# Kernel optimization log

Measured on AMD Instinct MI355X. Metric: run time of the kernel, lower is better.

The kernel has to match this reference:

```python
import jax, jax.numpy as jnp
import numpy as np

N = 50000      # ncount
IN_CH = 256    # in_channels
OUT_CH = 128   # out_channels
NNZ = 800000   # nnz per sparse matrix (avg degree 16)


def _spmm(rows, cols, vals, dense, n_rows):
    # sparse(COO) @ dense : gather rows of dense by col index, scale, scatter-add by row
    contrib = vals[:, None] * dense[cols]              # [nnz, F]
    return jax.ops.segment_sum(contrib, rows, num_segments=n_rows)


def setup_inputs() -> dict:
    key = jax.random.key(0)
    ks = jax.random.split(key, 12)
    phi_indices = jnp.stack([
        jax.random.randint(ks[0], (NNZ,), 0, N),
        jax.random.randint(ks[1], (NNZ,), 0, N)])
    phi_values = jax.random.normal(ks[2], (NNZ,), dtype=jnp.float32)
    phi_inverse_indices = jnp.stack([
        jax.random.randint(ks[3], (NNZ,), 0, N),
        jax.random.randint(ks[4], (NNZ,), 0, N)])
    phi_inverse_values = jax.random.normal(ks[5], (NNZ,), dtype=jnp.float32)
    feature_indices = jnp.stack([
        jax.random.randint(ks[6], (NNZ,), 0, N),       # node index
        jax.random.randint(ks[7], (NNZ,), 0, IN_CH)])  # feature column
    feature_values = jax.random.normal(ks[8], (NNZ,), dtype=jnp.float32)
    # xavier_uniform for weight_matrix
    limit = float(np.sqrt(6.0 / (IN_CH + OUT_CH)))
    weight_matrix = jax.random.uniform(ks[9], (IN_CH, OUT_CH), jnp.float32, -limit, limit)
    # diagonal filter Theta init uniform(0.9, 1.1)
    diagonal_weight_filter = jax.random.uniform(ks[10], (N,), jnp.float32, 0.9, 1.1)
    return {
        "phi_indices": phi_indices,
        "phi_values": phi_values,
        "phi_inverse_indices": phi_inverse_indices,
        "phi_inverse_values": phi_inverse_values,
        "feature_indices": feature_indices,
        "feature_values": feature_values,
        "weight_matrix": weight_matrix,
        "diagonal_weight_filter": diagonal_weight_filter,
        "dropout": 0,
    }


def reference(phi_indices, phi_values, phi_inverse_indices, phi_inverse_values,
              feature_indices, feature_values, weight_matrix,
              diagonal_weight_filter, dropout):
    # rescaled_phi = phi @ diag(theta): scales column j of phi by theta[j]
    scaled_phi_vals = phi_values * diagonal_weight_filter[phi_indices[1]]
    # filtered = features(sparse N x IN) @ W  -> [N, OUT]
    filtered = _spmm(feature_indices[0], feature_indices[1], feature_values,
                     weight_matrix, N)
    # (phi * D * phi_inv) @ filtered computed associatively without dense N x N:
    tmp = _spmm(phi_inverse_indices[0], phi_inverse_indices[1],
                phi_inverse_values, filtered, N)              # phi_inv @ filtered
    localized = _spmm(phi_indices[0], phi_indices[1],
                      scaled_phi_vals, tmp, N)                # (phi D) @ tmp
    # dropout in eval mode (training=False) is identity
    return jax.nn.relu(localized)
```

## Files before the change

### kernel.cpp

```cpp
#include <hip/hip_runtime.h>
#include <hip/hip_fp16.h>


#define OUT_CH 128
#define HALF_CH 64
#define RPB 256
#define RPB_SHIFT 8
#define MAX_NB 256
#define EPB 4096
#define EPT 16
#define MAX_CHUNK 16
#define STAGE_CAP 8192


__global__ __launch_bounds__(256) void bucket_hist_kernel(
    const int* __restrict__ rows0, int n0,
    const int* __restrict__ rows1, int n1,
    const int* __restrict__ rows2, int n2,
    int* __restrict__ hist_part,
    int NB, int NBLK)
{
    int m = blockIdx.y;
    const int* rows = (m == 0) ? rows0 : (m == 1) ? rows1 : rows2;
    int nnz         = (m == 0) ? n0    : (m == 1) ? n1    : n2;
    __shared__ int bins[MAX_NB];
    if (threadIdx.x < NB) bins[threadIdx.x] = 0;
    __syncthreads();
    int base = blockIdx.x * EPB;
    #pragma unroll 4
    for (int k = 0; k < EPB / 256; ++k) {
        int i = base + k * 256 + threadIdx.x;
        if (i < nnz) atomicAdd(&bins[rows[i] >> RPB_SHIFT], 1);
    }
    __syncthreads();
    int* out = hist_part + ((size_t)(m * NBLK + blockIdx.x)) * NB;
    if (threadIdx.x < NB) out[threadIdx.x] = bins[threadIdx.x];
}


__global__ __launch_bounds__(256) void scan_blocks_wave_kernel(
    int* __restrict__ hist_part, int* __restrict__ totals, int NB, int NBLK)
{
    int w = blockIdx.x * 4 + (threadIdx.x >> 6);
    if (w >= 3 * NB) return;
    int lane = threadIdx.x & 63;
    int m = w / NB, b = w - m * NB;
    const int chunk = (NBLK + 63) >> 6;
    int base_blk = lane * chunk;

    int v[MAX_CHUNK];
    int sum = 0;
    for (int k = 0; k < chunk; ++k) {
        int blk = base_blk + k;
        int x = (blk < NBLK) ? hist_part[((size_t)(m * NBLK + blk)) * NB + b] : 0;
        v[k] = x; sum += x;
    }
    int incl = sum;
    #pragma unroll
    for (int s = 1; s < 64; s <<= 1) {
        int y = __shfl_up(incl, s);
        if (lane >= s) incl += y;
    }
    int run = incl - sum;
    for (int k = 0; k < chunk; ++k) {
        int blk = base_blk + k;
        if (blk < NBLK) {
            hist_part[((size_t)(m * NBLK + blk)) * NB + b] = run;
            run += v[k];
        }
    }
    if (lane == 63) totals[w] = incl;
}


__global__ __launch_bounds__(1024) void scan_buckets_kernel(
    const int* __restrict__ totals, int* __restrict__ bases, int NB)
{
    int m = blockIdx.x;
    int t = threadIdx.x;
    int x = (t < NB) ? totals[m * NB + t] : 0;
    int lane = t & 63, wid = t >> 6;
    int incl = x;
    #pragma unroll
    for (int s = 1; s < 64; s <<= 1) {
        int y = __shfl_up(incl, s);
        if (lane >= s) incl += y;
    }
    __shared__ int wtot[16];
    __shared__ int wbase[16];
    if (lane == 63) wtot[wid] = incl;
    __syncthreads();
    if (t == 0) {
        int run = 0;
        #pragma unroll
        for (int w = 0; w < 16; ++w) { int v = wtot[w]; wbase[w] = run; run += v; }
    }
    __syncthreads();
    if (t < NB) bases[m * NB + t] = wbase[wid] + incl - x;
}


__global__ __launch_bounds__(256) void bucket_scatter_kernel(
    const int* __restrict__ rows0, const int* __restrict__ cols0, const float* __restrict__ vals0, int n0,
    const int* __restrict__ rows1, const int* __restrict__ cols1, const float* __restrict__ vals1, int n1,
    const int* __restrict__ rows2, const int* __restrict__ cols2, const float* __restrict__ vals2, int n2,
    const float* __restrict__ theta,
    const int* __restrict__ hist_part, const int* __restrict__ bases,
    int2* __restrict__ eb0, int2* __restrict__ eb1, int2* __restrict__ eb2,
    int NB, int NBLK)
{
    int m = blockIdx.y;
    const int* rows; const int* cols; const float* vals; int nnz; int2* eb;
    if (m == 0)      { rows = rows0; cols = cols0; vals = vals0; nnz = n0; eb = eb0; }
    else if (m == 1) { rows = rows1; cols = cols1; vals = vals1; nnz = n1; eb = eb1; }
    else             { rows = rows2; cols = cols2; vals = vals2; nnz = n2; eb = eb2; }

    __shared__ int2 staged[EPB];
    __shared__ unsigned char bucket_of[EPB];
    __shared__ int lhist[MAX_NB];
    __shared__ int lstart[MAX_NB + 1];
    __shared__ int lcur[MAX_NB];
    __shared__ int gbase[MAX_NB];
    __shared__ int wtot[4], wbase[4];

    int t = threadIdx.x;
    if (t < NB) lhist[t] = 0;
    __syncthreads();

    int base = blockIdx.x * EPB;
    bool fold = (m == 2);

    int  bk[EPT];
    int2 pl[EPT];
    #pragma unroll
    for (int k = 0; k < EPT; ++k) {
        int i = base + k * 256 + t;
        if (i < nnz) {
            int r = rows[i], c = cols[i];
            float v = vals[i];
            if (fold) v *= theta[c];
            bk[k] = r >> RPB_SHIFT;
            pl[k] = make_int2(c | ((r & (RPB - 1)) << 16), __float_as_int(v));
            atomicAdd(&lhist[bk[k]], 1);
        } else bk[k] = -1;
    }
    __syncthreads();

    {
        int x = (t < NB) ? lhist[t] : 0;
        int lane = t & 63, wid = t >> 6;
        int incl = x;
        #pragma unroll
        for (int s = 1; s < 64; s <<= 1) {
            int y = __shfl_up(incl, s);
            if (lane >= s) incl += y;
        }
        if (lane == 63) wtot[wid] = incl;
        __syncthreads();
        if (t == 0) {
            int run = 0;
            #pragma unroll
            for (int w = 0; w < 4; ++w) { int v = wtot[w]; wbase[w] = run; run += v; }
            lstart[MAX_NB] = run;
        }
        __syncthreads();
        if (t < NB) {
            int excl = wbase[wid] + incl - x;
            lstart[t] = excl;
            lcur[t]   = excl;
            const int* hp = hist_part + ((size_t)(m * NBLK + blockIdx.x)) * NB;
            gbase[t] = bases[m * NB + t] + hp[t];
        }
    }
    __syncthreads();

    #pragma unroll
    for (int k = 0; k < EPT; ++k) {
        if (bk[k] >= 0) {
            int idx = atomicAdd(&lcur[bk[k]], 1);
            staged[idx] = pl[k];
            bucket_of[idx] = (unsigned char)bk[k];
        }
    }
    __syncthreads();

    int count = min(EPB, nnz - base);
    for (int i = t; i < count; i += 256) {
        int b = bucket_of[i];
        int dest = gbase[b] + (i - lstart[b]);
        eb[dest] = staged[i];
    }
}


__global__ __launch_bounds__(256) void bucket_to_csr_kernel(
    const int2* __restrict__ eb0, const int2* __restrict__ eb1, const int2* __restrict__ eb2,
    unsigned int* __restrict__ ec0, unsigned int* __restrict__ ec1, unsigned int* __restrict__ ec2,
    const int* __restrict__ bases,
    int* __restrict__ off,
    int n0, int n1, int n2, int NB, int n)
{
    int m = blockIdx.y;
    int b = blockIdx.x;
    const int2* eb; unsigned int* ec; int nnz;
    if (m == 0)      { eb = eb0; ec = ec0; nnz = n0; }
    else if (m == 1) { eb = eb1; ec = ec1; nnz = n1; }
    else             { eb = eb2; ec = ec2; nnz = n2; }
    int base = bases[m * NB + b];
    int end  = (b + 1 < NB) ? bases[m * NB + b + 1] : nnz;
    int cnt  = end - base;

    __shared__ unsigned int staged_c[STAGE_CAP];
    __shared__ int hist[RPB];
    __shared__ int cur[RPB];
    __shared__ int loc[RPB + 1];
    __shared__ int wtot[4];
    __shared__ int wbase[4];
    int t = threadIdx.x;
    hist[t] = 0; cur[t] = 0;
    __syncthreads();
    for (int i = base + t; i < end; i += 256)
        atomicAdd(&hist[(eb[i].x >> 16) & (RPB - 1)], 1);
    __syncthreads();
    {
        int x = hist[t];
        int lane = t & 63, wid = t >> 6;
        int incl = x;
        #pragma unroll
        for (int s = 1; s < 64; s <<= 1) {
            int y = __shfl_up(incl, s);
            if (lane >= s) incl += y;
        }
        if (lane == 63) wtot[wid] = incl;
        __syncthreads();
        if (t == 0) {
            int run = 0;
            #pragma unroll
            for (int w = 0; w < 4; ++w) { int v = wtot[w]; wbase[w] = run; run += v; }
        }
        __syncthreads();
        loc[t] = wbase[wid] + incl - x;
        if (t == RPB - 1) loc[RPB] = wbase[3] + incl;
    }
    __syncthreads();
    {
        int r = b * RPB + t;
        if (r <= n) off[(size_t)m * (n + 1) + r] = base + loc[t];
        if (b == NB - 1 && t == 0) off[(size_t)m * (n + 1) + n] = nnz;
    }
    if (cnt <= STAGE_CAP) {
        for (int i = base + t; i < end; i += 256) {
            int2 e = eb[i];
            int rl = (e.x >> 16) & (RPB - 1);
            int rk = atomicAdd(&cur[rl], 1);
            unsigned short h = __half_as_ushort(__float2half_rn(__int_as_float(e.y)));
            staged_c[loc[rl] + rk] = (unsigned int)(e.x & 0xFFFF) | ((unsigned int)h << 16);
        }
        __syncthreads();
        for (int i = t; i < cnt; i += 256)
            ec[base + i] = staged_c[i];
    } else {
        for (int i = base + t; i < end; i += 256) {
            int2 e = eb[i];
            int rl = (e.x >> 16) & (RPB - 1);
            int rk = atomicAdd(&cur[rl], 1);
            unsigned short h = __half_as_ushort(__float2half_rn(__int_as_float(e.y)));
            ec[base + loc[rl] + rk] = (unsigned int)(e.x & 0xFFFF) | ((unsigned int)h << 16);
        }
    }
}


template<bool SRC_H, bool DST_H, bool RELU>
__global__ __launch_bounds__(256) void spmm_csr_kernel(
    const int* __restrict__ off, const unsigned int* __restrict__ edges,
    const void* __restrict__ dense_v, void* __restrict__ out_v, int nrows)
{
    int lane = threadIdx.x & 63;
    int r = blockIdx.x * 4 + (threadIdx.x >> 6);
    if (r >= nrows) return;
    int j   = __builtin_amdgcn_readfirstlane(off[r]);
    int end = __builtin_amdgcn_readfirstlane(off[r + 1]);
    const float2*  df = (const float2*)dense_v;
    const __half2* dh = (const __half2*)dense_v;

    float2 a0 = make_float2(0.f, 0.f), a1 = make_float2(0.f, 0.f);

    for (; j + 8 <= end; j += 8) {
        unsigned int e[8]; float2 d[8];
        #pragma unroll
        for (int k = 0; k < 8; ++k) e[k] = edges[j + k];
        #pragma unroll
        for (int k = 0; k < 8; ++k) {
            if (SRC_H) d[k] = __half22float2(dh[(size_t)(e[k] & 0xFFFF) * HALF_CH + lane]);
            else       d[k] = df[(size_t)(e[k] & 0xFFFF) * HALF_CH + lane];
        }
        #pragma unroll
        for (int k = 0; k < 8; ++k) {
            float v = __half2float(__ushort_as_half((unsigned short)(e[k] >> 16)));
            if (k & 1) { a1.x = fmaf(v, d[k].x, a1.x); a1.y = fmaf(v, d[k].y, a1.y); }
            else       { a0.x = fmaf(v, d[k].x, a0.x); a0.y = fmaf(v, d[k].y, a0.y); }
        }
    }
    for (; j + 4 <= end; j += 4) {
        unsigned int e[4]; float2 d[4];
        #pragma unroll
        for (int k = 0; k < 4; ++k) e[k] = edges[j + k];
        #pragma unroll
        for (int k = 0; k < 4; ++k) {
            if (SRC_H) d[k] = __half22float2(dh[(size_t)(e[k] & 0xFFFF) * HALF_CH + lane]);
            else       d[k] = df[(size_t)(e[k] & 0xFFFF) * HALF_CH + lane];
        }
        #pragma unroll
        for (int k = 0; k < 4; ++k) {
            float v = __half2float(__ushort_as_half((unsigned short)(e[k] >> 16)));
            if (k & 1) { a1.x = fmaf(v, d[k].x, a1.x); a1.y = fmaf(v, d[k].y, a1.y); }
            else       { a0.x = fmaf(v, d[k].x, a0.x); a0.y = fmaf(v, d[k].y, a0.y); }
        }
    }
    for (; j < end; ++j) {
        unsigned int e0 = edges[j];
        float2 d0;
        if (SRC_H) d0 = __half22float2(dh[(size_t)(e0 & 0xFFFF) * HALF_CH + lane]);
        else       d0 = df[(size_t)(e0 & 0xFFFF) * HALF_CH + lane];
        float v0 = __half2float(__ushort_as_half((unsigned short)(e0 >> 16)));
        a0.x = fmaf(v0, d0.x, a0.x); a0.y = fmaf(v0, d0.y, a0.y);
    }
    float2 res = make_float2(a0.x + a1.x, a0.y + a1.y);
    if (RELU) { res.x = fmaxf(res.x, 0.f); res.y = fmaxf(res.y, 0.f); }
    if (DST_H) ((__half2*)out_v)[(size_t)r * HALF_CH + lane] = __float22half2_rn(res);
    else       ((float2*) out_v)[(size_t)r * HALF_CH + lane] = res;
}


__global__ __launch_bounds__(256) void spmm_atomic_kernel(
    const int* __restrict__ rows, const int* __restrict__ cols,
    const float* __restrict__ vals, const float* __restrict__ theta,
    const float* __restrict__ dense, float* __restrict__ out, int nnz)
{
    int idx = blockIdx.x * blockDim.x + threadIdx.x;
    int e = idx >> 7;
    int f = idx & (OUT_CH - 1);
    if (e >= nnz) return;
    int r = rows[e];
    int c = cols[e];
    float v = vals[e];
    if (theta != nullptr) v *= theta[c];
    atomicAdd(&out[(size_t)r * OUT_CH + f], v * dense[(size_t)c * OUT_CH + f]);
}

__global__ __launch_bounds__(256) void relu_kernel(float* __restrict__ out, int n4)
{
    int i = blockIdx.x * blockDim.x + threadIdx.x;
    if (i >= n4) return;
    float4 v = ((float4*)out)[i];
    v.x = fmaxf(v.x, 0.f); v.y = fmaxf(v.y, 0.f);
    v.z = fmaxf(v.z, 0.f); v.w = fmaxf(v.w, 0.f);
    ((float4*)out)[i] = v;
}


static inline size_t align16(size_t x) { return (x + 15) & ~(size_t)15; }

extern "C" void kernel_launch(void* const* d_in, const int* in_sizes, int n_in,
                              void* d_out, int out_size, void* d_ws, size_t ws_size,
                              hipStream_t stream)
{
    const int*   phi_idx   = (const int*)d_in[0];
    const float* phi_vals  = (const float*)d_in[1];
    const int*   phii_idx  = (const int*)d_in[2];
    const float* phii_vals = (const float*)d_in[3];
    const int*   feat_idx  = (const int*)d_in[4];
    const float* feat_vals = (const float*)d_in[5];
    const float* W         = (const float*)d_in[6];
    const float* theta     = (const float*)d_in[7];

    const int nnz_phi  = in_sizes[1];
    const int nnz_phii = in_sizes[3];
    const int nnz_feat = in_sizes[5];
    const int n_nodes  = in_sizes[7];
    const int in_ch    = in_sizes[6] / OUT_CH;
    const size_t dense_elems = (size_t)n_nodes * OUT_CH;
    const long long total_e = (long long)nnz_feat + nnz_phii + nnz_phi;

    const int NB = (n_nodes + RPB - 1) >> RPB_SHIFT;
    int max_nnz = nnz_feat > nnz_phii ? nnz_feat : nnz_phii;
    if (nnz_phi > max_nnz) max_nnz = nnz_phi;
    const int NBLK = (max_nnz + EPB - 1) / EPB;

    size_t p = 0;
    size_t filtered_off = p; p += align16(dense_elems * sizeof(__half));
    size_t tmp_off      = p; p += align16(dense_elems * sizeof(__half));
    size_t off_off      = p; p += align16((size_t)3 * (n_nodes + 1) * sizeof(int));
    size_t hp_off       = p; p += align16((size_t)3 * NBLK * NB * sizeof(int));
    size_t tot_off      = p; p += align16((size_t)3 * NB * sizeof(int));
    size_t bas_off      = p; p += align16((size_t)3 * NB * sizeof(int));
    size_t eb_off       = p; p += align16((size_t)total_e * sizeof(int2));
    size_t ec_off       = p; p += align16((size_t)total_e * sizeof(unsigned int));
    size_t need = p;

    char* ws = (char*)d_ws;
    dim3 block(256);

    bool fast_ok = (ws_size >= need) && (NB <= MAX_NB) && (n_nodes <= 65536) &&
                   (in_ch <= 65536) && (NBLK <= 64 * MAX_CHUNK);

    if (fast_ok) {
        __half* filtered = (__half*)(ws + filtered_off);
        __half* tmp      = (__half*)(ws + tmp_off);
        int* off_arr    = (int*)(ws + off_off);
        int* hist_part  = (int*)(ws + hp_off);
        int* totals     = (int*)(ws + tot_off);
        int* bases      = (int*)(ws + bas_off);
        int2* eb0 = (int2*)(ws + eb_off);
        int2* eb1 = eb0 + nnz_feat;
        int2* eb2 = eb1 + nnz_phii;
        unsigned int* ec0 = (unsigned int*)(ws + ec_off);
        unsigned int* ec1 = ec0 + nnz_feat;
        unsigned int* ec2 = ec1 + nnz_phii;

        const int* rows0 = feat_idx;  const int* cols0 = feat_idx + nnz_feat;
        const int* rows1 = phii_idx;  const int* cols1 = phii_idx + nnz_phii;
        const int* rows2 = phi_idx;   const int* cols2 = phi_idx  + nnz_phi;

        bucket_hist_kernel<<<dim3(NBLK, 3), block, 0, stream>>>(
            rows0, nnz_feat, rows1, nnz_phii, rows2, nnz_phi,
            hist_part, NB, NBLK);

        int nwaves = 3 * NB;
        scan_blocks_wave_kernel<<<dim3((nwaves + 3) / 4), block, 0, stream>>>(
            hist_part, totals, NB, NBLK);

        scan_buckets_kernel<<<dim3(3), dim3(1024), 0, stream>>>(totals, bases, NB);

        bucket_scatter_kernel<<<dim3(NBLK, 3), block, 0, stream>>>(
            rows0, cols0, feat_vals, nnz_feat,
            rows1, cols1, phii_vals, nnz_phii,
            rows2, cols2, phi_vals,  nnz_phi,
            theta, hist_part, bases, eb0, eb1, eb2, NB, NBLK);

        bucket_to_csr_kernel<<<dim3(NB, 3), block, 0, stream>>>(
            eb0, eb1, eb2, ec0, ec1, ec2, bases, off_arr,
            nnz_feat, nnz_phii, nnz_phi, NB, n_nodes);

        int* off_f  = off_arr;
        int* off_pi = off_arr + (n_nodes + 1);
        int* off_p  = off_arr + 2 * (n_nodes + 1);

        dim3 grid_r((unsigned)((n_nodes + 3) / 4));
        spmm_csr_kernel<false, true, false><<<grid_r, block, 0, stream>>>(
            off_f,  ec0, (const void*)W, (void*)filtered, n_nodes);
        spmm_csr_kernel<true, true, false><<<grid_r, block, 0, stream>>>(
            off_pi, ec1, (const void*)filtered, (void*)tmp, n_nodes);
        spmm_csr_kernel<true, false, true><<<grid_r, block, 0, stream>>>(
            off_p,  ec2, (const void*)tmp, d_out, n_nodes);
    } else {
        float* filtered = (float*)ws;
        float* tmp      = filtered + dense_elems;
        hipMemsetAsync(filtered, 0, 2 * dense_elems * sizeof(float), stream);
        hipMemsetAsync(d_out, 0, (size_t)out_size * sizeof(float), stream);
        {
            long long t = (long long)nnz_feat * OUT_CH;
            spmm_atomic_kernel<<<dim3((unsigned)((t + 255) / 256)), block, 0, stream>>>(
                feat_idx, feat_idx + nnz_feat, feat_vals, nullptr, W, filtered, nnz_feat);
        }
        {
            long long t = (long long)nnz_phii * OUT_CH;
            spmm_atomic_kernel<<<dim3((unsigned)((t + 255) / 256)), block, 0, stream>>>(
                phii_idx, phii_idx + nnz_phii, phii_vals, nullptr, filtered, tmp, nnz_phii);
        }
        {
            long long t = (long long)nnz_phi * OUT_CH;
            spmm_atomic_kernel<<<dim3((unsigned)((t + 255) / 256)), block, 0, stream>>>(
                phi_idx, phi_idx + nnz_phi, phi_vals, theta, tmp, (float*)d_out, nnz_phi);
        }
        {
            int n4 = out_size / 4;
            relu_kernel<<<dim3((n4 + 255) / 256), block, 0, stream>>>((float*)d_out, n4);
        }
    }
}
```

Baseline: 218.6 us.

## Split bucket entries into key and fp16 value arrays, use per-wave histograms

```diff
diff --git a/kernel.cpp b/kernel.cpp
--- a/kernel.cpp
+++ b/kernel.cpp
@@ -23,18 +23,20 @@
     int m = blockIdx.y;
     const int* rows = (m == 0) ? rows0 : (m == 1) ? rows1 : rows2;
     int nnz         = (m == 0) ? n0    : (m == 1) ? n1    : n2;
-    __shared__ int bins[MAX_NB];
-    if (threadIdx.x < NB) bins[threadIdx.x] = 0;
+    __shared__ int bins[4][MAX_NB];
+    int t = threadIdx.x;
+    int wid = t >> 6;
+    for (int i = t; i < 4 * MAX_NB; i += 256) ((int*)bins)[i] = 0;
     __syncthreads();
     int base = blockIdx.x * EPB;
     #pragma unroll 4
     for (int k = 0; k < EPB / 256; ++k) {
-        int i = base + k * 256 + threadIdx.x;
-        if (i < nnz) atomicAdd(&bins[rows[i] >> RPB_SHIFT], 1);
+        int i = base + k * 256 + t;
+        if (i < nnz) atomicAdd(&bins[wid][rows[i] >> RPB_SHIFT], 1);
     }
     __syncthreads();
     int* out = hist_part + ((size_t)(m * NBLK + blockIdx.x)) * NB;
-    if (threadIdx.x < NB) out[threadIdx.x] = bins[threadIdx.x];
+    if (t < NB) out[t] = bins[0][t] + bins[1][t] + bins[2][t] + bins[3][t];
 }
 
 
@@ -106,32 +108,37 @@
     const int* __restrict__ rows2, const int* __restrict__ cols2, const float* __restrict__ vals2, int n2,
     const float* __restrict__ theta,
     const int* __restrict__ hist_part, const int* __restrict__ bases,
-    int2* __restrict__ eb0, int2* __restrict__ eb1, int2* __restrict__ eb2,
+    unsigned int* __restrict__ ek0, unsigned int* __restrict__ ek1, unsigned int* __restrict__ ek2,
+    unsigned short* __restrict__ ev0, unsigned short* __restrict__ ev1, unsigned short* __restrict__ ev2,
     int NB, int NBLK)
 {
     int m = blockIdx.y;
-    const int* rows; const int* cols; const float* vals; int nnz; int2* eb;
-    if (m == 0)      { rows = rows0; cols = cols0; vals = vals0; nnz = n0; eb = eb0; }
-    else if (m == 1) { rows = rows1; cols = cols1; vals = vals1; nnz = n1; eb = eb1; }
-    else             { rows = rows2; cols = cols2; vals = vals2; nnz = n2; eb = eb2; }
-
-    __shared__ int2 staged[EPB];
-    __shared__ unsigned char bucket_of[EPB];
-    __shared__ int lhist[MAX_NB];
-    __shared__ int lstart[MAX_NB + 1];
+    const int* rows; const int* cols; const float* vals; int nnz;
+    unsigned int* ek; unsigned short* ev;
+    if (m == 0)      { rows = rows0; cols = cols0; vals = vals0; nnz = n0; ek = ek0; ev = ev0; }
+    else if (m == 1) { rows = rows1; cols = cols1; vals = vals1; nnz = n1; ek = ek1; ev = ev1; }
+    else             { rows = rows2; cols = cols2; vals = vals2; nnz = n2; ek = ek2; ev = ev2; }
+
+    __shared__ unsigned int   skey[EPB];
+    __shared__ unsigned short sval[EPB];
+    __shared__ unsigned char  bucket_of[EPB];
+    __shared__ int lhist[4][MAX_NB];
+    __shared__ int lstart[MAX_NB];
     __shared__ int lcur[MAX_NB];
     __shared__ int gbase[MAX_NB];
     __shared__ int wtot[4], wbase[4];
 
     int t = threadIdx.x;
-    if (t < NB) lhist[t] = 0;
+    int wid = t >> 6;
+    for (int i = t; i < 4 * MAX_NB; i += 256) ((int*)lhist)[i] = 0;
     __syncthreads();
 
     int base = blockIdx.x * EPB;
     bool fold = (m == 2);
 
-    int  bk[EPT];
-    int2 pl[EPT];
+    int bk[EPT];
+    unsigned int   pk[EPT];
+    unsigned short pv[EPT];
     #pragma unroll
     for (int k = 0; k < EPT; ++k) {
         int i = base + k * 256 + t;
@@ -140,15 +147,17 @@
             float v = vals[i];
             if (fold) v *= theta[c];
             bk[k] = r >> RPB_SHIFT;
-            pl[k] = make_int2(c | ((r & (RPB - 1)) << 16), __float_as_int(v));
-            atomicAdd(&lhist[bk[k]], 1);
+            pk[k] = (unsigned int)c | ((unsigned int)(r & (RPB - 1)) << 16);
+            pv[k] = __half_as_ushort(__float2half_rn(v));
+            atomicAdd(&lhist[wid][bk[k]], 1);
         } else bk[k] = -1;
     }
     __syncthreads();
 
     {
-        int x = (t < NB) ? lhist[t] : 0;
-        int lane = t & 63, wid = t >> 6;
+        int x = 0;
+        if (t < NB) x = lhist[0][t] + lhist[1][t] + lhist[2][t] + lhist[3][t];
+        int lane = t & 63;
         int incl = x;
         #pragma unroll
         for (int s = 1; s < 64; s <<= 1) {
@@ -161,7 +170,6 @@
             int run = 0;
             #pragma unroll
             for (int w = 0; w < 4; ++w) { int v = wtot[w]; wbase[w] = run; run += v; }
-            lstart[MAX_NB] = run;
         }
         __syncthreads();
         if (t < NB) {
@@ -178,7 +186,8 @@
     for (int k = 0; k < EPT; ++k) {
         if (bk[k] >= 0) {
             int idx = atomicAdd(&lcur[bk[k]], 1);
-            staged[idx] = pl[k];
+            skey[idx] = pk[k];
+            sval[idx] = pv[k];
             bucket_of[idx] = (unsigned char)bk[k];
         }
     }
@@ -188,13 +197,15 @@
     for (int i = t; i < count; i += 256) {
         int b = bucket_of[i];
         int dest = gbase[b] + (i - lstart[b]);
-        eb[dest] = staged[i];
+        ek[dest] = skey[i];
+        ev[dest] = sval[i];
     }
 }
 
 
 __global__ __launch_bounds__(256) void bucket_to_csr_kernel(
-    const int2* __restrict__ eb0, const int2* __restrict__ eb1, const int2* __restrict__ eb2,
+    const unsigned int* __restrict__ ek0, const unsigned int* __restrict__ ek1, const unsigned int* __restrict__ ek2,
+    const unsigned short* __restrict__ ev0, const unsigned short* __restrict__ ev1, const unsigned short* __restrict__ ev2,
     unsigned int* __restrict__ ec0, unsigned int* __restrict__ ec1, unsigned int* __restrict__ ec2,
     const int* __restrict__ bases,
     int* __restrict__ off,
@@ -202,29 +213,31 @@
 {
     int m = blockIdx.y;
     int b = blockIdx.x;
-    const int2* eb; unsigned int* ec; int nnz;
-    if (m == 0)      { eb = eb0; ec = ec0; nnz = n0; }
-    else if (m == 1) { eb = eb1; ec = ec1; nnz = n1; }
-    else             { eb = eb2; ec = ec2; nnz = n2; }
+    const unsigned int* ek; const unsigned short* ev; unsigned int* ec; int nnz;
+    if (m == 0)      { ek = ek0; ev = ev0; ec = ec0; nnz = n0; }
+    else if (m == 1) { ek = ek1; ev = ev1; ec = ec1; nnz = n1; }
+    else             { ek = ek2; ev = ev2; ec = ec2; nnz = n2; }
     int base = bases[m * NB + b];
     int end  = (b + 1 < NB) ? bases[m * NB + b + 1] : nnz;
     int cnt  = end - base;
 
     __shared__ unsigned int staged_c[STAGE_CAP];
-    __shared__ int hist[RPB];
+    __shared__ int histw[4][RPB];
     __shared__ int cur[RPB];
     __shared__ int loc[RPB + 1];
     __shared__ int wtot[4];
     __shared__ int wbase[4];
     int t = threadIdx.x;
-    hist[t] = 0; cur[t] = 0;
+    int wid = t >> 6;
+    for (int i = t; i < 4 * RPB; i += 256) ((int*)histw)[i] = 0;
+    cur[t] = 0;
     __syncthreads();
     for (int i = base + t; i < end; i += 256)
-        atomicAdd(&hist[(eb[i].x >> 16) & (RPB - 1)], 1);
+        atomicAdd(&histw[wid][(ek[i] >> 16) & (RPB - 1)], 1);
     __syncthreads();
     {
-        int x = hist[t];
-        int lane = t & 63, wid = t >> 6;
+        int x = histw[0][t] + histw[1][t] + histw[2][t] + histw[3][t];
+        int lane = t & 63;
         int incl = x;
         #pragma unroll
         for (int s = 1; s < 64; s <<= 1) {
@@ -250,22 +263,20 @@
     }
     if (cnt <= STAGE_CAP) {
         for (int i = base + t; i < end; i += 256) {
-            int2 e = eb[i];
-            int rl = (e.x >> 16) & (RPB - 1);
+            unsigned int k = ek[i];
+            int rl = (k >> 16) & (RPB - 1);
             int rk = atomicAdd(&cur[rl], 1);
-            unsigned short h = __half_as_ushort(__float2half_rn(__int_as_float(e.y)));
-            staged_c[loc[rl] + rk] = (unsigned int)(e.x & 0xFFFF) | ((unsigned int)h << 16);
+            staged_c[loc[rl] + rk] = (k & 0xFFFFu) | ((unsigned int)ev[i] << 16);
         }
         __syncthreads();
         for (int i = t; i < cnt; i += 256)
             ec[base + i] = staged_c[i];
     } else {
         for (int i = base + t; i < end; i += 256) {
-            int2 e = eb[i];
-            int rl = (e.x >> 16) & (RPB - 1);
+            unsigned int k = ek[i];
+            int rl = (k >> 16) & (RPB - 1);
             int rk = atomicAdd(&cur[rl], 1);
-            unsigned short h = __half_as_ushort(__float2half_rn(__int_as_float(e.y)));
-            ec[base + loc[rl] + rk] = (unsigned int)(e.x & 0xFFFF) | ((unsigned int)h << 16);
+            ec[base + loc[rl] + rk] = (k & 0xFFFFu) | ((unsigned int)ev[i] << 16);
         }
     }
 }
@@ -395,7 +406,8 @@
     size_t hp_off       = p; p += align16((size_t)3 * NBLK * NB * sizeof(int));
     size_t tot_off      = p; p += align16((size_t)3 * NB * sizeof(int));
     size_t bas_off      = p; p += align16((size_t)3 * NB * sizeof(int));
-    size_t eb_off       = p; p += align16((size_t)total_e * sizeof(int2));
+    size_t ek_off       = p; p += align16((size_t)total_e * sizeof(unsigned int));
+    size_t ev_off       = p; p += align16((size_t)total_e * sizeof(unsigned short));
     size_t ec_off       = p; p += align16((size_t)total_e * sizeof(unsigned int));
     size_t need = p;
 
@@ -412,12 +424,15 @@
         int* hist_part  = (int*)(ws + hp_off);
         int* totals     = (int*)(ws + tot_off);
         int* bases      = (int*)(ws + bas_off);
-        int2* eb0 = (int2*)(ws + eb_off);
-        int2* eb1 = eb0 + nnz_feat;
-        int2* eb2 = eb1 + nnz_phii;
-        unsigned int* ec0 = (unsigned int*)(ws + ec_off);
-        unsigned int* ec1 = ec0 + nnz_feat;
-        unsigned int* ec2 = ec1 + nnz_phii;
+        unsigned int*   ek0 = (unsigned int*)(ws + ek_off);
+        unsigned int*   ek1 = ek0 + nnz_feat;
+        unsigned int*   ek2 = ek1 + nnz_phii;
+        unsigned short* ev0 = (unsigned short*)(ws + ev_off);
+        unsigned short* ev1 = ev0 + nnz_feat;
+        unsigned short* ev2 = ev1 + nnz_phii;
+        unsigned int*   ec0 = (unsigned int*)(ws + ec_off);
+        unsigned int*   ec1 = ec0 + nnz_feat;
+        unsigned int*   ec2 = ec1 + nnz_phii;
 
         const int* rows0 = feat_idx;  const int* cols0 = feat_idx + nnz_feat;
         const int* rows1 = phii_idx;  const int* cols1 = phii_idx + nnz_phii;
@@ -437,10 +452,11 @@
             rows0, cols0, feat_vals, nnz_feat,
             rows1, cols1, phii_vals, nnz_phii,
             rows2, cols2, phi_vals,  nnz_phi,
-            theta, hist_part, bases, eb0, eb1, eb2, NB, NBLK);
+            theta, hist_part, bases,
+            ek0, ek1, ek2, ev0, ev1, ev2, NB, NBLK);
 
         bucket_to_csr_kernel<<<dim3(NB, 3), block, 0, stream>>>(
-            eb0, eb1, eb2, ec0, ec1, ec2, bases, off_arr,
+            ek0, ek1, ek2, ev0, ev1, ev2, ec0, ec1, ec2, bases, off_arr,
             nnz_feat, nnz_phii, nnz_phi, NB, n_nodes);
 
         int* off_f  = off_arr;
```

Result: slower. 224.7 us (+2.7%).
